# Performance work log

Measured on AMD Instinct MI355X. Metric: run time of the kernel, lower is better.

## Reference

```python
import jax, jax.numpy as jnp
import numpy as np

N_HEAD = 16
ROPE_BASE = 10000.0


def _rope_tables(T, head_dim, dtype):
    inv_freq = 1.0 / (ROPE_BASE ** (jnp.arange(0, head_dim, 2, dtype=jnp.float32) / head_dim))
    t = jnp.arange(T, dtype=jnp.float32)
    freqs = t[:, None] * inv_freq[None, :]          # [T, hd/2]
    emb = jnp.concatenate([freqs, freqs], axis=-1)  # [T, hd]
    return jnp.cos(emb).astype(dtype), jnp.sin(emb).astype(dtype)


def _rotate_half(x):
    h = x.shape[-1] // 2
    return jnp.concatenate([-x[..., h:], x[..., :h]], axis=-1)


def setup_inputs() -> dict:
    key = jax.random.key(0)
    k1, k2, k3 = jax.random.split(key, 3)
    B, T, C = 2, 2048, 1024
    x = jax.random.normal(k1, (B, T, C), dtype=jnp.float32)
    w_attn = jax.random.normal(k2, (3 * C, C), dtype=jnp.float32) * (1.0 / np.sqrt(C))
    w_proj = jax.random.normal(k3, (C, C), dtype=jnp.float32) * (1.0 / np.sqrt(C))
    return {"x": x, "w_attn": w_attn, "w_proj": w_proj}


def reference(x, w_attn, w_proj):
    B, T, C = x.shape
    H = N_HEAD
    hd = C // H

    qkv = jnp.einsum('btc,fc->btf', x, w_attn)          # [B,T,3C]
    q, k, v = jnp.split(qkv, 3, axis=-1)
    # [B,H,T,hd]
    q = q.reshape(B, T, H, hd).transpose(0, 2, 1, 3)
    k = k.reshape(B, T, H, hd).transpose(0, 2, 1, 3)
    v = v.reshape(B, T, H, hd).transpose(0, 2, 1, 3)

    cos, sin = _rope_tables(T, hd, x.dtype)             # [T,hd]
    cos = cos[None, None]
    sin = sin[None, None]
    q = q * cos + _rotate_half(q) * sin
    k = k * cos + _rotate_half(k) * sin

    scale = 1.0 / np.sqrt(hd)
    scores = jnp.einsum('bhqd,bhkd->bhqk', q, k) * scale  # [B,H,T,T]
    causal = jnp.tril(jnp.ones((T, T), dtype=bool))
    scores = jnp.where(causal[None, None], scores, jnp.finfo(scores.dtype).min)
    attn = jax.nn.softmax(scores, axis=-1)
    out = jnp.einsum('bhqk,bhkd->bhqd', attn, v)          # [B,H,T,hd]
    out = out.transpose(0, 2, 1, 3).reshape(B, T, C)
    return jnp.einsum('btc,oc->bto', out, w_proj)
```

## Files before the change

### kernel.cpp

```cpp
#include <hip/hip_runtime.h>
#include <hip/hip_bf16.h>
#include <stdint.h>

typedef unsigned short u16;
typedef __bf16 bf16x8 __attribute__((ext_vector_type(8)));
typedef float f32x4 __attribute__((ext_vector_type(4)));

#define B_ 2
#define T_ 2048
#define C_ 1024
#define H_ 16
#define HD 64
#define M_ (B_ * T_)
#define N3 (3 * C_)

__device__ __forceinline__ float bf2f(u16 u) {
  return __uint_as_float(((unsigned int)u) << 16);
}
__device__ __forceinline__ u16 f2bf(float f) {
  unsigned int u = __float_as_uint(f);
  u += 0x7FFF + ((u >> 16) & 1);
  return (u16)(u >> 16);
}
__device__ __forceinline__ unsigned cvt_pk_bf16(float lo, float hi) {
  unsigned r;
  asm("v_cvt_pk_bf16_f32 %0, %1, %2" : "=v"(r) : "v"(lo), "v"(hi));
  return r;
}
__device__ __forceinline__ void async16(void* ldsp, const void* gp) {
  __builtin_amdgcn_global_load_lds(
      (const __attribute__((address_space(1))) unsigned int*)gp,
      (__attribute__((address_space(3))) unsigned int*)ldsp, 16, 0, 0);
}

union U16x8 { uint4 v; u16 u[8]; };

__device__ __forceinline__ bf16x8 ldsAfrag(const char* base, int row, int kbyte) {
  int off = (row * 128 + kbyte) ^ ((row & 7) << 4);
  uint4 t = *reinterpret_cast<const uint4*>(base + off);
  return __builtin_bit_cast(bf16x8, t);
}
__device__ __forceinline__ bf16x8 ldsRead(const char* p) {
  uint4 t = *reinterpret_cast<const uint4*>(p);
  return __builtin_bit_cast(bf16x8, t);
}

__global__ void cvt_bf16(const float* __restrict__ src, u16* __restrict__ dst, int n4) {
  int i = blockIdx.x * blockDim.x + threadIdx.x;
  int stride = gridDim.x * blockDim.x;
  for (; i < n4; i += stride) {
    float4 v = reinterpret_cast<const float4*>(src)[i];
    uint2 o;
    o.x = (unsigned)f2bf(v.x) | ((unsigned)f2bf(v.y) << 16);
    o.y = (unsigned)f2bf(v.z) | ((unsigned)f2bf(v.w) << 16);
    reinterpret_cast<uint2*>(dst)[i] = o;
  }
}

__global__ void rope_tables_kernel(float* __restrict__ cosT, float* __restrict__ sinT) {
  int t = blockIdx.x;
  int i = threadIdx.x;
  float inv = powf(10000.0f, -(float)i * (1.0f / 32.0f));
  float f = (float)t * inv;
  cosT[t * 32 + i] = cosf(f);
  sinT[t * 32 + i] = sinf(f);
}

template <bool OUT_F32>
__global__ __launch_bounds__(256) void gemm_bt(const u16* __restrict__ A,
                                               const u16* __restrict__ Bw,
                                               void* __restrict__ Cout,
                                               int M, int N, int K) {
  __shared__ uint4 ldsbuf[2048];
  char* As = (char*)ldsbuf;
  char* Bs = (char*)ldsbuf + 16384;
  const int tid = threadIdx.x;
  const int lane = tid & 63;
  const int wv = tid >> 6;
  const int wr = wv >> 1, wc = wv & 1;
  const int lrow = lane & 15, lgrp = lane >> 4;
  const long m0 = (long)blockIdx.x * 128, n0 = (long)blockIdx.y * 128;
  const int srow_l = lane >> 3;
  const int csrc = ((lane & 7) ^ (lane >> 3)) * 8;
  f32x4 acc[4][4] = {};
  for (int k0 = 0; k0 < K; k0 += 64) {
    __syncthreads();
#pragma unroll
    for (int p = 0; p < 4; ++p) {
      int seg = wv * 4 + p;
      int row = seg * 8 + srow_l;
      async16(As + seg * 1024, A + (size_t)(m0 + row) * K + k0 + csrc);
      async16(Bs + seg * 1024, Bw + (size_t)(n0 + row) * K + k0 + csrc);
    }
    __syncthreads();
#pragma unroll
    for (int ks = 0; ks < 2; ++ks) {
      bf16x8 af[4], bfr[4];
#pragma unroll
      for (int i = 0; i < 4; ++i) {
        af[i]  = ldsAfrag(As, wr * 64 + i * 16 + lrow, ks * 64 + lgrp * 16);
        bfr[i] = ldsAfrag(Bs, wc * 64 + i * 16 + lrow, ks * 64 + lgrp * 16);
      }
#pragma unroll
      for (int i = 0; i < 4; ++i)
#pragma unroll
        for (int j = 0; j < 4; ++j)
          acc[i][j] = __builtin_amdgcn_mfma_f32_16x16x32_bf16(af[i], bfr[j], acc[i][j], 0, 0, 0);
    }
  }
#pragma unroll
  for (int i = 0; i < 4; ++i)
#pragma unroll
    for (int j = 0; j < 4; ++j) {
      long r0 = m0 + wr * 64 + i * 16 + lgrp * 4;
      long c  = n0 + wc * 64 + j * 16 + lrow;
#pragma unroll
      for (int r = 0; r < 4; ++r) {
        float v = acc[i][j][r];
        if (OUT_F32)
          ((float*)Cout)[(r0 + r) * N + c] = v;
        else
          ((u16*)Cout)[(r0 + r) * N + c] = f2bf(v);
      }
    }
}

__global__ __launch_bounds__(256) void rope_reshape(const u16* __restrict__ qkv,
                                                    const float* __restrict__ cosT,
                                                    const float* __restrict__ sinT,
                                                    u16* __restrict__ Q,
                                                    u16* __restrict__ K,
                                                    u16* __restrict__ Vt) {
  __shared__ u16 Vs[64][80];
  const float SCLQ = 0.125f * 1.4426950408889634f;
  const int tid = threadIdx.x;
  const int tblk = blockIdx.x, bh = blockIdx.y;
  const int b = bh >> 4, h = bh & 15;
  const int tl = tid >> 2, quar = tid & 3;
  const int t = tblk * 64 + tl;
  const u16* rowp = qkv + ((size_t)(b * T_ + t)) * N3 + h * HD;
  const int d0 = quar * 8;
  float cs[8], sn[8];
#pragma unroll
  for (int j = 0; j < 8; ++j) {
    cs[j] = cosT[t * 32 + d0 + j];
    sn[j] = sinT[t * 32 + d0 + j];
  }
#pragma unroll
  for (int part = 0; part < 2; ++part) {
    const u16* p = rowp + part * C_;
    U16x8 x1, x2, o1, o2;
    x1.v = *reinterpret_cast<const uint4*>(p + d0);
    x2.v = *reinterpret_cast<const uint4*>(p + d0 + 32);
#pragma unroll
    for (int j = 0; j < 8; ++j) {
      float a = bf2f(x1.u[j]), c2 = bf2f(x2.u[j]);
      float f1 = a * cs[j] - c2 * sn[j];
      float f2 = c2 * cs[j] + a * sn[j];
      if (part == 0) { f1 *= SCLQ; f2 *= SCLQ; }
      o1.u[j] = f2bf(f1);
      o2.u[j] = f2bf(f2);
    }
    u16* dst = (part ? K : Q) + ((size_t)bh * T_ + t) * HD;
    *reinterpret_cast<uint4*>(dst + d0) = o1.v;
    *reinterpret_cast<uint4*>(dst + d0 + 32) = o2.v;
  }
  const u16* pv = rowp + 2 * C_;
#pragma unroll
  for (int c = 0; c < 2; ++c) {
    int d = quar * 16 + c * 8;
    *reinterpret_cast<uint4*>(&Vs[tl][d]) = *reinterpret_cast<const uint4*>(pv + d);
  }
  __syncthreads();
  const int d = tid >> 2, tq = tid & 3;
  U16x8 a, bv;
#pragma unroll
  for (int j = 0; j < 8; ++j) a.u[j] = Vs[tq * 16 + j][d];
#pragma unroll
  for (int j = 0; j < 8; ++j) bv.u[j] = Vs[tq * 16 + 8 + j][d];
  u16* dstv = Vt + ((size_t)bh * HD + d) * T_ + tblk * 64 + tq * 16;
  *reinterpret_cast<uint4*>(dstv) = a.v;
  *reinterpret_cast<uint4*>(dstv + 8) = bv.v;
}

__global__ __launch_bounds__(256) void attn_fwd12(const u16* __restrict__ Q,
                                                  const u16* __restrict__ K,
                                                  const u16* __restrict__ Vt,
                                                  u16* __restrict__ O) {
  __shared__ uint4 lds4[3072];
  char* ldsb = (char*)lds4;
  const int tid = threadIdx.x;
  const int lane = tid & 63, wv = tid >> 6;
  const int lrow = lane & 15, lgrp = lane >> 4;
  const int bh = blockIdx.y;
  const int b = bh >> 4, h = bh & 15;
  const u16* Qh = Q + (size_t)bh * T_ * HD;
  const u16* Kh = K + (size_t)bh * T_ * HD;
  const u16* Vh = Vt + (size_t)bh * HD * T_;

  const int srow_l = lane >> 3;
  const int csrc = ((lane & 7) ^ (lane >> 3)) * 8;

  auto stage = [&](int slot, int kt) {
    char* Kd = ldsb + (slot << 14);
    char* Vd = Kd + 8192;
    const u16* Kg = Kh + (size_t)(kt * 64) * HD;
    const u16* Vg = Vh + kt * 64;
#pragma unroll
    for (int seg = 0; seg < 2; ++seg) {
      int row = wv * 16 + seg * 8 + srow_l;
      async16(Kd + wv * 2048 + seg * 1024, Kg + (size_t)row * HD + csrc);
      async16(Vd + wv * 2048 + seg * 1024, Vg + (size_t)row * T_ + csrc);
    }
  };

  const int swz = (lrow & 7) << 4;
  const int krA = lrow * 128 + ((lgrp * 16) ^ swz);
  const int krB = lrow * 128 + ((64 + lgrp * 16) ^ swz);
  const int vrA = 8192 + krA;
  const int vrB = 8192 + krB;
  char* PsW = ldsb + 32768 + wv * 4096 + lrow * 128;
  char* pw0 = PsW + ((0 * 32 + lgrp * 8) ^ swz);
  char* pw1 = PsW + ((1 * 32 + lgrp * 8) ^ swz);
  char* pw2 = PsW + ((2 * 32 + lgrp * 8) ^ swz);
  char* pw3 = PsW + ((3 * 32 + lgrp * 8) ^ swz);
  const char* paA = PsW + ((lgrp * 16) ^ swz);
  const char* paB = PsW + ((64 + lgrp * 16) ^ swz);

  uint4 ones4;
  ones4.x = ones4.y = ones4.z = ones4.w = 0x3F803F80u;
  const bf16x8 ones8 = __builtin_bit_cast(bf16x8, ones4);

  const int unit = 15 - (int)blockIdx.x;
  const int q0 = unit * 128;
  const int qg0 = q0 + wv * 32 + lrow;
  const int qg1 = qg0 + 16;
  const int nu = unit * 2 + 2;

  bf16x8 qf[2][2];
#pragma unroll
  for (int m = 0; m < 2; ++m)
#pragma unroll
    for (int ks = 0; ks < 2; ++ks) {
      uint4 t4 = *reinterpret_cast<const uint4*>(
          Qh + (size_t)(q0 + wv * 32 + m * 16 + lrow) * HD + ks * 32 + lgrp * 8);
      qf[m][ks] = __builtin_bit_cast(bf16x8, t4);
    }
  f32x4 o[2][4] = {};
  f32x4 lacc[2] = {};

  stage(0, 0);
  __syncthreads();

  int cur = 0;
  for (int kt = 0; kt < nu; ++kt) {
    if (kt + 1 < nu) stage(cur ^ 1, kt + 1);
    const char* buf = ldsb + (cur << 14);
    const char* KbA = buf + krA;
    const char* KbB = buf + krB;
    const char* VbA = buf + vrA;
    const char* VbB = buf + vrB;

    f32x4 s[2][4] = {};
    __builtin_amdgcn_s_setprio(1);
#pragma unroll
    for (int n = 0; n < 4; ++n) {
      bf16x8 bk = ldsRead(KbA + n * 2048);
      s[0][n] = __builtin_amdgcn_mfma_f32_16x16x32_bf16(bk, qf[0][0], s[0][n], 0, 0, 0);
      s[1][n] = __builtin_amdgcn_mfma_f32_16x16x32_bf16(bk, qf[1][0], s[1][n], 0, 0, 0);
    }
#pragma unroll
    for (int n = 0; n < 4; ++n) {
      bf16x8 bk = ldsRead(KbB + n * 2048);
      s[0][n] = __builtin_amdgcn_mfma_f32_16x16x32_bf16(bk, qf[0][1], s[0][n], 0, 0, 0);
      s[1][n] = __builtin_amdgcn_mfma_f32_16x16x32_bf16(bk, qf[1][1], s[1][n], 0, 0, 0);
    }
    __builtin_amdgcn_s_setprio(0);

    if (kt >= nu - 2) {
#pragma unroll
      for (int n = 0; n < 4; ++n)
#pragma unroll
        for (int r = 0; r < 4; ++r) {
          int kg = kt * 64 + n * 16 + lgrp * 4 + r;
          s[0][n][r] = exp2f((kg <= qg0) ? s[0][n][r] : -__builtin_inff());
          s[1][n][r] = exp2f((kg <= qg1) ? s[1][n][r] : -__builtin_inff());
        }
    } else {
#pragma unroll
      for (int n = 0; n < 4; ++n)
#pragma unroll
        for (int r = 0; r < 4; ++r) {
          s[0][n][r] = exp2f(s[0][n][r]);
          s[1][n][r] = exp2f(s[1][n][r]);
        }
    }

#pragma unroll
    for (int m = 0; m < 2; ++m) {
      uint2 w0, w1, w2, w3;
      w0.x = cvt_pk_bf16(s[m][0][0], s[m][0][1]); w0.y = cvt_pk_bf16(s[m][0][2], s[m][0][3]);
      w1.x = cvt_pk_bf16(s[m][1][0], s[m][1][1]); w1.y = cvt_pk_bf16(s[m][1][2], s[m][1][3]);
      w2.x = cvt_pk_bf16(s[m][2][0], s[m][2][1]); w2.y = cvt_pk_bf16(s[m][2][2], s[m][2][3]);
      w3.x = cvt_pk_bf16(s[m][3][0], s[m][3][1]); w3.y = cvt_pk_bf16(s[m][3][2], s[m][3][3]);
      *reinterpret_cast<uint2*>(pw0 + m * 2048) = w0;
      *reinterpret_cast<uint2*>(pw1 + m * 2048) = w1;
      *reinterpret_cast<uint2*>(pw2 + m * 2048) = w2;
      *reinterpret_cast<uint2*>(pw3 + m * 2048) = w3;
    }

    __builtin_amdgcn_s_setprio(1);
#pragma unroll
    for (int ks = 0; ks < 2; ++ks) {
      const char* pab = ks ? paB : paA;
      bf16x8 pa0 = ldsRead(pab);
      bf16x8 pa1 = ldsRead(pab + 2048);
      lacc[0] = __builtin_amdgcn_mfma_f32_16x16x32_bf16(pa0, ones8, lacc[0], 0, 0, 0);
      lacc[1] = __builtin_amdgcn_mfma_f32_16x16x32_bf16(pa1, ones8, lacc[1], 0, 0, 0);
      const char* vbb = ks ? VbB : VbA;
#pragma unroll
      for (int dn = 0; dn < 4; ++dn) {
        bf16x8 bv = ldsRead(vbb + dn * 2048);
        o[0][dn] = __builtin_amdgcn_mfma_f32_16x16x32_bf16(pa0, bv, o[0][dn], 0, 0, 0);
        o[1][dn] = __builtin_amdgcn_mfma_f32_16x16x32_bf16(pa1, bv, o[1][dn], 0, 0, 0);
      }
    }
    __builtin_amdgcn_s_setprio(0);
    __syncthreads();
    cur ^= 1;
  }

#pragma unroll
  for (int m = 0; m < 2; ++m)
#pragma unroll
    for (int r = 0; r < 4; ++r) {
      float inv = 1.0f / lacc[m][r];
      int t = q0 + wv * 32 + m * 16 + lgrp * 4 + r;
#pragma unroll
      for (int dn = 0; dn < 4; ++dn) {
        int c = h * HD + dn * 16 + lrow;
        O[((size_t)(b * T_ + t)) * C_ + c] = f2bf(o[m][dn][r] * inv);
      }
    }
}

extern "C" void kernel_launch(void* const* d_in, const int* in_sizes, int n_in,
                              void* d_out, int out_size, void* d_ws, size_t ws_size,
                              hipStream_t stream) {
  const float* x  = (const float*)d_in[0];
  const float* wa = (const float*)d_in[1];
  const float* wp = (const float*)d_in[2];
  float* out = (float*)d_out;
  char* ws = (char*)d_ws;
  size_t off = 0;
  auto alloc = [&](size_t bytes) {
    char* p = ws + off;
    off += (bytes + 255) & ~(size_t)255;
    return p;
  };
  u16* xb   = (u16*)alloc((size_t)M_ * C_ * 2);
  u16* wab  = (u16*)alloc((size_t)N3 * C_ * 2);
  u16* wpb  = (u16*)alloc((size_t)C_ * C_ * 2);
  u16* qkvb = (u16*)alloc((size_t)M_ * N3 * 2);
  u16* Qb   = (u16*)alloc((size_t)B_ * H_ * T_ * HD * 2);
  u16* Kb   = (u16*)alloc((size_t)B_ * H_ * T_ * HD * 2);
  u16* Vtb  = (u16*)alloc((size_t)B_ * H_ * T_ * HD * 2);
  u16* Ob   = (u16*)alloc((size_t)M_ * C_ * 2);
  float* cosT = (float*)alloc((size_t)T_ * 32 * 4);
  float* sinT = (float*)alloc((size_t)T_ * 32 * 4);
  (void)in_sizes; (void)n_in; (void)out_size; (void)ws_size;

  cvt_bf16<<<1024, 256, 0, stream>>>(x, xb, M_ * C_ / 4);
  cvt_bf16<<<1024, 256, 0, stream>>>(wa, wab, N3 * C_ / 4);
  cvt_bf16<<<512, 256, 0, stream>>>(wp, wpb, C_ * C_ / 4);
  rope_tables_kernel<<<T_, 32, 0, stream>>>(cosT, sinT);
  gemm_bt<false><<<dim3(M_ / 128, N3 / 128), 256, 0, stream>>>(xb, wab, qkvb, M_, N3, C_);
  rope_reshape<<<dim3(T_ / 64, B_ * H_), 256, 0, stream>>>(qkvb, cosT, sinT, Qb, Kb, Vtb);
  attn_fwd12<<<dim3(16, B_ * H_), 256, 0, stream>>>(Qb, Kb, Vtb, Ob);
  gemm_bt<true><<<dim3(M_ / 128, C_ / 128), 256, 0, stream>>>(Ob, wpb, out, M_, C_, C_);
}
```

Measured before the change: 145.4 us.

## Split attention into single-wave blocks with 32-row query tiles and no barriers

```diff
diff --git a/kernel.cpp b/kernel.cpp
--- a/kernel.cpp
+++ b/kernel.cpp
@@ -13,6 +13,8 @@
 #define HD 64
 #define M_ (B_ * T_)
 #define N3 (3 * C_)
+
+#define WAITV(N) asm volatile("s_waitcnt vmcnt(" #N ")" ::: "memory")
 
 __device__ __forceinline__ float bf2f(u16 u) {
   return __uint_as_float(((unsigned int)u) << 16);
@@ -183,14 +185,15 @@
   *reinterpret_cast<uint4*>(dstv + 8) = bv.v;
 }
 
-__global__ __launch_bounds__(256) void attn_fwd12(const u16* __restrict__ Q,
-                                                  const u16* __restrict__ K,
-                                                  const u16* __restrict__ Vt,
-                                                  u16* __restrict__ O) {
-  __shared__ uint4 lds4[3072];
+__global__ __launch_bounds__(64)
+__attribute__((amdgpu_waves_per_eu(2, 2)))
+void attn_fwd14(const u16* __restrict__ Q,
+                const u16* __restrict__ K,
+                const u16* __restrict__ Vt,
+                u16* __restrict__ O) {
+  __shared__ uint4 lds4[1152];
   char* ldsb = (char*)lds4;
-  const int tid = threadIdx.x;
-  const int lane = tid & 63, wv = tid >> 6;
+  const int lane = threadIdx.x & 63;
   const int lrow = lane & 15, lgrp = lane >> 4;
   const int bh = blockIdx.y;
   const int b = bh >> 4, h = bh & 15;
@@ -198,44 +201,46 @@
   const u16* Kh = K + (size_t)bh * T_ * HD;
   const u16* Vh = Vt + (size_t)bh * HD * T_;
 
-  const int srow_l = lane >> 3;
-  const int csrc = ((lane & 7) ^ (lane >> 3)) * 8;
+  const int sx = (lane & 7) ^ (lane >> 3);
+  const int krow_l = lane >> 3;
+  const u16* Ksrc = Kh + (size_t)krow_l * HD + sx * 8;
+  const int vd_l = krow_l + ((sx >> 2) << 5);
+  const int vkc = (sx & 3) * 8;
 
   auto stage = [&](int slot, int kt) {
-    char* Kd = ldsb + (slot << 14);
-    char* Vd = Kd + 8192;
-    const u16* Kg = Kh + (size_t)(kt * 64) * HD;
-    const u16* Vg = Vh + kt * 64;
-#pragma unroll
-    for (int seg = 0; seg < 2; ++seg) {
-      int row = wv * 16 + seg * 8 + srow_l;
-      async16(Kd + wv * 2048 + seg * 1024, Kg + (size_t)row * HD + csrc);
-      async16(Vd + wv * 2048 + seg * 1024, Vg + (size_t)row * T_ + csrc);
+    char* Kd = ldsb + slot * 8192;
+    char* Vd = Kd + 4096;
+    const u16* Kg = Ksrc + (size_t)(kt * 32) * HD;
+    const u16* Vg = Vh + kt * 32 + vkc;
+#pragma unroll
+    for (int seg = 0; seg < 4; ++seg) {
+      async16(Kd + seg * 1024, Kg + (size_t)(seg * 8) * HD);
+      async16(Vd + seg * 1024, Vg + (size_t)(seg * 8 + vd_l) * T_);
     }
   };
 
   const int swz = (lrow & 7) << 4;
   const int krA = lrow * 128 + ((lgrp * 16) ^ swz);
   const int krB = lrow * 128 + ((64 + lgrp * 16) ^ swz);
-  const int vrA = 8192 + krA;
-  const int vrB = 8192 + krB;
-  char* PsW = ldsb + 32768 + wv * 4096 + lrow * 128;
-  char* pw0 = PsW + ((0 * 32 + lgrp * 8) ^ swz);
-  char* pw1 = PsW + ((1 * 32 + lgrp * 8) ^ swz);
-  char* pw2 = PsW + ((2 * 32 + lgrp * 8) ^ swz);
-  char* pw3 = PsW + ((3 * 32 + lgrp * 8) ^ swz);
-  const char* paA = PsW + ((lgrp * 16) ^ swz);
-  const char* paB = PsW + ((64 + lgrp * 16) ^ swz);
+  const int vrA = 4096 + lrow * 128 + ((lgrp * 16) ^ swz);
+  const int vrB = 4096 + lrow * 128 + ((64 + lgrp * 16) ^ swz);
+  char* Pb = ldsb + 16384;
+  char* pw00 = Pb + lrow * 128 + (((0 * 64 + 0 * 32 + lgrp * 8)) ^ swz);
+  char* pw01 = Pb + lrow * 128 + (((0 * 64 + 1 * 32 + lgrp * 8)) ^ swz);
+  char* pw10 = Pb + lrow * 128 + (((1 * 64 + 0 * 32 + lgrp * 8)) ^ swz);
+  char* pw11 = Pb + lrow * 128 + (((1 * 64 + 1 * 32 + lgrp * 8)) ^ swz);
+  const char* pa0 = Pb + lrow * 128 + ((lgrp * 16) ^ swz);
+  const char* pa1 = Pb + lrow * 128 + ((64 + lgrp * 16) ^ swz);
 
   uint4 ones4;
   ones4.x = ones4.y = ones4.z = ones4.w = 0x3F803F80u;
   const bf16x8 ones8 = __builtin_bit_cast(bf16x8, ones4);
 
-  const int unit = 15 - (int)blockIdx.x;
-  const int q0 = unit * 128;
-  const int qg0 = q0 + wv * 32 + lrow;
+  const int c = 63 - (int)blockIdx.x;
+  const int qs = c * 32;
+  const int nu = c + 1;
+  const int qg0 = qs + lrow;
   const int qg1 = qg0 + 16;
-  const int nu = unit * 2 + 2;
 
   bf16x8 qf[2][2];
 #pragma unroll
@@ -243,52 +248,52 @@
 #pragma unroll
     for (int ks = 0; ks < 2; ++ks) {
       uint4 t4 = *reinterpret_cast<const uint4*>(
-          Qh + (size_t)(q0 + wv * 32 + m * 16 + lrow) * HD + ks * 32 + lgrp * 8);
+          Qh + (size_t)(qs + m * 16 + lrow) * HD + ks * 32 + lgrp * 8);
       qf[m][ks] = __builtin_bit_cast(bf16x8, t4);
     }
   f32x4 o[2][4] = {};
   f32x4 lacc[2] = {};
 
   stage(0, 0);
-  __syncthreads();
-
-  int cur = 0;
+
   for (int kt = 0; kt < nu; ++kt) {
-    if (kt + 1 < nu) stage(cur ^ 1, kt + 1);
-    const char* buf = ldsb + (cur << 14);
-    const char* KbA = buf + krA;
-    const char* KbB = buf + krB;
-    const char* VbA = buf + vrA;
-    const char* VbB = buf + vrB;
-
-    f32x4 s[2][4] = {};
+    const char* buf = ldsb + (kt & 1) * 8192;
+    if (kt + 1 < nu) {
+      stage((kt + 1) & 1, kt + 1);
+      WAITV(8);
+    } else {
+      WAITV(0);
+    }
+    __builtin_amdgcn_sched_barrier(0);
+
+    f32x4 s[2][2] = {};
     __builtin_amdgcn_s_setprio(1);
 #pragma unroll
-    for (int n = 0; n < 4; ++n) {
-      bf16x8 bk = ldsRead(KbA + n * 2048);
+    for (int n = 0; n < 2; ++n) {
+      bf16x8 bk = ldsRead(buf + krA + n * 2048);
       s[0][n] = __builtin_amdgcn_mfma_f32_16x16x32_bf16(bk, qf[0][0], s[0][n], 0, 0, 0);
       s[1][n] = __builtin_amdgcn_mfma_f32_16x16x32_bf16(bk, qf[1][0], s[1][n], 0, 0, 0);
     }
 #pragma unroll
-    for (int n = 0; n < 4; ++n) {
-      bf16x8 bk = ldsRead(KbB + n * 2048);
+    for (int n = 0; n < 2; ++n) {
+      bf16x8 bk = ldsRead(buf + krB + n * 2048);
       s[0][n] = __builtin_amdgcn_mfma_f32_16x16x32_bf16(bk, qf[0][1], s[0][n], 0, 0, 0);
       s[1][n] = __builtin_amdgcn_mfma_f32_16x16x32_bf16(bk, qf[1][1], s[1][n], 0, 0, 0);
     }
     __builtin_amdgcn_s_setprio(0);
 
-    if (kt >= nu - 2) {
-#pragma unroll
-      for (int n = 0; n < 4; ++n)
+    if (kt == nu - 1) {
+#pragma unroll
+      for (int n = 0; n < 2; ++n)
 #pragma unroll
         for (int r = 0; r < 4; ++r) {
-          int kg = kt * 64 + n * 16 + lgrp * 4 + r;
+          int kg = kt * 32 + n * 16 + lgrp * 4 + r;
           s[0][n][r] = exp2f((kg <= qg0) ? s[0][n][r] : -__builtin_inff());
           s[1][n][r] = exp2f((kg <= qg1) ? s[1][n][r] : -__builtin_inff());
         }
     } else {
 #pragma unroll
-      for (int n = 0; n < 4; ++n)
+      for (int n = 0; n < 2; ++n)
 #pragma unroll
         for (int r = 0; r < 4; ++r) {
           s[0][n][r] = exp2f(s[0][n][r]);
@@ -297,37 +302,30 @@
     }
 
 #pragma unroll
-    for (int m = 0; m < 2; ++m) {
-      uint2 w0, w1, w2, w3;
-      w0.x = cvt_pk_bf16(s[m][0][0], s[m][0][1]); w0.y = cvt_pk_bf16(s[m][0][2], s[m][0][3]);
-      w1.x = cvt_pk_bf16(s[m][1][0], s[m][1][1]); w1.y = cvt_pk_bf16(s[m][1][2], s[m][1][3]);
-      w2.x = cvt_pk_bf16(s[m][2][0], s[m][2][1]); w2.y = cvt_pk_bf16(s[m][2][2], s[m][2][3]);
-      w3.x = cvt_pk_bf16(s[m][3][0], s[m][3][1]); w3.y = cvt_pk_bf16(s[m][3][2], s[m][3][3]);
-      *reinterpret_cast<uint2*>(pw0 + m * 2048) = w0;
-      *reinterpret_cast<uint2*>(pw1 + m * 2048) = w1;
-      *reinterpret_cast<uint2*>(pw2 + m * 2048) = w2;
-      *reinterpret_cast<uint2*>(pw3 + m * 2048) = w3;
+    for (int n = 0; n < 2; ++n) {
+      uint2 w0, w1;
+      w0.x = cvt_pk_bf16(s[0][n][0], s[0][n][1]);
+      w0.y = cvt_pk_bf16(s[0][n][2], s[0][n][3]);
+      w1.x = cvt_pk_bf16(s[1][n][0], s[1][n][1]);
+      w1.y = cvt_pk_bf16(s[1][n][2], s[1][n][3]);
+      *reinterpret_cast<uint2*>(n ? pw01 : pw00) = w0;
+      *reinterpret_cast<uint2*>(n ? pw11 : pw10) = w1;
     }
 
     __builtin_amdgcn_s_setprio(1);
-#pragma unroll
-    for (int ks = 0; ks < 2; ++ks) {
-      const char* pab = ks ? paB : paA;
-      bf16x8 pa0 = ldsRead(pab);
-      bf16x8 pa1 = ldsRead(pab + 2048);
-      lacc[0] = __builtin_amdgcn_mfma_f32_16x16x32_bf16(pa0, ones8, lacc[0], 0, 0, 0);
-      lacc[1] = __builtin_amdgcn_mfma_f32_16x16x32_bf16(pa1, ones8, lacc[1], 0, 0, 0);
-      const char* vbb = ks ? VbB : VbA;
+    {
+      bf16x8 p0 = ldsRead(pa0);
+      bf16x8 p1 = ldsRead(pa1);
+      lacc[0] = __builtin_amdgcn_mfma_f32_16x16x32_bf16(p0, ones8, lacc[0], 0, 0, 0);
+      lacc[1] = __builtin_amdgcn_mfma_f32_16x16x32_bf16(p1, ones8, lacc[1], 0, 0, 0);
 #pragma unroll
       for (int dn = 0; dn < 4; ++dn) {
-        bf16x8 bv = ldsRead(vbb + dn * 2048);
-        o[0][dn] = __builtin_amdgcn_mfma_f32_16x16x32_bf16(pa0, bv, o[0][dn], 0, 0, 0);
-        o[1][dn] = __builtin_amdgcn_mfma_f32_16x16x32_bf16(pa1, bv, o[1][dn], 0, 0, 0);
+        bf16x8 bv = ldsRead(buf + (dn >> 1 ? vrB : vrA) + (dn & 1) * 2048);
+        o[0][dn] = __builtin_amdgcn_mfma_f32_16x16x32_bf16(p0, bv, o[0][dn], 0, 0, 0);
+        o[1][dn] = __builtin_amdgcn_mfma_f32_16x16x32_bf16(p1, bv, o[1][dn], 0, 0, 0);
       }
     }
     __builtin_amdgcn_s_setprio(0);
-    __syncthreads();
-    cur ^= 1;
   }
 
 #pragma unroll
@@ -335,11 +333,11 @@
 #pragma unroll
     for (int r = 0; r < 4; ++r) {
       float inv = 1.0f / lacc[m][r];
-      int t = q0 + wv * 32 + m * 16 + lgrp * 4 + r;
+      int t = qs + m * 16 + lgrp * 4 + r;
 #pragma unroll
       for (int dn = 0; dn < 4; ++dn) {
-        int c = h * HD + dn * 16 + lrow;
-        O[((size_t)(b * T_ + t)) * C_ + c] = f2bf(o[m][dn][r] * inv);
+        int col = h * HD + dn * 16 + lrow;
+        O[((size_t)(b * T_ + t)) * C_ + col] = f2bf(o[m][dn][r] * inv);
       }
     }
 }
@@ -376,6 +374,6 @@
   rope_tables_kernel<<<T_, 32, 0, stream>>>(cosT, sinT);
   gemm_bt<false><<<dim3(M_ / 128, N3 / 128), 256, 0, stream>>>(xb, wab, qkvb, M_, N3, C_);
   rope_reshape<<<dim3(T_ / 64, B_ * H_), 256, 0, stream>>>(qkvb, cosT, sinT, Qb, Kb, Vtb);
-  attn_fwd12<<<dim3(16, B_ * H_), 256, 0, stream>>>(Qb, Kb, Vtb, Ob);
+  attn_fwd14<<<dim3(64, B_ * H_), 64, 0, stream>>>(Qb, Kb, Vtb, Ob);
   gemm_bt<true><<<dim3(M_ / 128, C_ / 128), 256, 0, stream>>>(Ob, wpb, out, M_, C_, C_);
 }
```

Result: slower. 154.2 us (+6.0%).
